# Kernel optimization log

Hardware: AMD Instinct MI355X
Metric: run time of the kernel (lower is better)

## Reference

```python
import jax, jax.numpy as jnp
import numpy as np

IN_F, OUT_F, N_PAIRS, BATCH = 1024, 1024, 4096, 32768
EPS = 1e-5

def setup_inputs() -> dict:
    key = jax.random.key(0)
    ks = jax.random.split(key, 8)
    x = jax.random.normal(ks[0], (BATCH, IN_F), dtype=jnp.float32)
    idx_i = jax.random.randint(ks[1], (N_PAIRS,), 0, IN_F)
    idx_j = jax.random.randint(ks[2], (N_PAIRS,), 0, IN_F)
    bound_lc = 1.0 / np.sqrt(N_PAIRS)
    bound_w1 = 1.0 / np.sqrt(IN_F)
    lw = jax.random.uniform(ks[3], (OUT_F, N_PAIRS), minval=-bound_lc, maxval=bound_lc, dtype=jnp.float32)
    w1 = jax.random.uniform(ks[4], (OUT_F, IN_F), minval=-bound_w1, maxval=bound_w1, dtype=jnp.float32)
    scale = jnp.ones((1, IN_F), dtype=jnp.float32)
    translation = jnp.zeros((1, IN_F), dtype=jnp.float32)
    gamma = jnp.ones((OUT_F,), dtype=jnp.float32)
    beta = jnp.zeros((OUT_F,), dtype=jnp.float32)
    return {"x": x, "idx_i": idx_i, "idx_j": idx_j, "scale": scale,
            "translation": translation, "lw": lw, "w1": w1,
            "gamma": gamma, "beta": beta}

def reference(x, idx_i, idx_j, scale, translation, lw, w1, gamma, beta):
    # levicivita transform: affine-normalize, gather pairs, multiply, GEMM
    xs = (x - translation) / scale                       # [B, in]
    pp = xs[:, idx_i] * xs[:, idx_j]                     # [B, num_pairs]
    lc = pp @ lw.T                                       # [B, out]
    base = x @ w1.T                                      # [B, out]
    c = lc + base
    # LayerNorm over last dim (eps=1e-5, biased variance, as torch)
    mu = jnp.mean(c, axis=-1, keepdims=True)
    var = jnp.mean(jnp.square(c - mu), axis=-1, keepdims=True)
    return (c - mu) * jax.lax.rsqrt(var + EPS) * gamma + beta
```

## Files before the change

kernel.cpp:

```cpp
#include <hip/hip_runtime.h>
#include <hip/hip_bf16.h>
#include <stdint.h>


#define IN_F 1024
#define OUT_F 1024
#define N_PAIRS 4096
#define BATCH_N 32768
#define KTOT (N_PAIRS + IN_F)
#define EPS_LN 1e-5f

#define BM 256
#define BN 256
#define BK 64
#define NKT (KTOT / BK)
#define RS ((size_t)KTOT * 2)

typedef __attribute__((ext_vector_type(8))) __bf16 bf16x8;
typedef __attribute__((ext_vector_type(4))) float f32x4;

__device__ __forceinline__ unsigned short f32_to_bf16_bits(float f) {
  union { float f; unsigned u; } c; c.f = f;
  unsigned r = c.u + 0x7FFFu + ((c.u >> 16) & 1u);
  return (unsigned short)(r >> 16);
}

__device__ __forceinline__ void gload_lds16(const void* g, void* l) {
  __builtin_amdgcn_global_load_lds(
      (const __attribute__((address_space(1))) void*)g,
      (__attribute__((address_space(3))) void*)l, 16, 0, 0);
}

__global__ __launch_bounds__(256) void prep_w_kernel(
    const float* __restrict__ lw, const float* __restrict__ w1,
    unsigned short* __restrict__ Wcat) {
  int t = blockIdx.x * 256 + threadIdx.x;
  int e = t * 4;
  int o = e / KTOT;
  int k = e - o * KTOT;
  const float* src = (k < N_PAIRS) ? (lw + (size_t)o * N_PAIRS + k)
                                   : (w1 + (size_t)o * IN_F + (k - N_PAIRS));
  float4 v = *reinterpret_cast<const float4*>(src);
  ushort4 b;
  b.x = f32_to_bf16_bits(v.x);
  b.y = f32_to_bf16_bits(v.y);
  b.z = f32_to_bf16_bits(v.z);
  b.w = f32_to_bf16_bits(v.w);
  *reinterpret_cast<ushort4*>(Wcat + e) = b;
}

__global__ __launch_bounds__(256) void prep_x_kernel(
    const float* __restrict__ x,
    const int* __restrict__ idx_i, const int* __restrict__ idx_j,
    const float* __restrict__ scale, const float* __restrict__ translation,
    unsigned short* __restrict__ Xcat, int rowBase) {
  __shared__ float xs[IN_F];
  int r = blockIdx.x;
  int t = threadIdx.x;
  const float* xrow = x + (size_t)(rowBase + r) * IN_F;
  float4 xv = reinterpret_cast<const float4*>(xrow)[t];
  float4 sv = reinterpret_cast<const float4*>(scale)[t];
  float4 tv = reinterpret_cast<const float4*>(translation)[t];
  float4 xsv;
  xsv.x = (xv.x - tv.x) / sv.x;
  xsv.y = (xv.y - tv.y) / sv.y;
  xsv.z = (xv.z - tv.z) / sv.z;
  xsv.w = (xv.w - tv.w) / sv.w;
  reinterpret_cast<float4*>(xs)[t] = xsv;

  unsigned short* rowout = Xcat + (size_t)r * KTOT;
  ushort4 xb;
  xb.x = f32_to_bf16_bits(xv.x);
  xb.y = f32_to_bf16_bits(xv.y);
  xb.z = f32_to_bf16_bits(xv.z);
  xb.w = f32_to_bf16_bits(xv.w);
  *reinterpret_cast<ushort4*>(rowout + N_PAIRS + t * 4) = xb;

  __syncthreads();
#pragma unroll
  for (int g = 0; g < 2; ++g) {
    int p = (g * 256 + t) * 8;
    int4 ia = *reinterpret_cast<const int4*>(idx_i + p);
    int4 ib = *reinterpret_cast<const int4*>(idx_i + p + 4);
    int4 ja = *reinterpret_cast<const int4*>(idx_j + p);
    int4 jb = *reinterpret_cast<const int4*>(idx_j + p + 4);
    ushort4 oa, ob;
    oa.x = f32_to_bf16_bits(xs[ia.x] * xs[ja.x]);
    oa.y = f32_to_bf16_bits(xs[ia.y] * xs[ja.y]);
    oa.z = f32_to_bf16_bits(xs[ia.z] * xs[ja.z]);
    oa.w = f32_to_bf16_bits(xs[ia.w] * xs[ja.w]);
    ob.x = f32_to_bf16_bits(xs[ib.x] * xs[jb.x]);
    ob.y = f32_to_bf16_bits(xs[ib.y] * xs[jb.y]);
    ob.z = f32_to_bf16_bits(xs[ib.z] * xs[jb.z]);
    ob.w = f32_to_bf16_bits(xs[ib.w] * xs[jb.w]);
    *reinterpret_cast<ushort4*>(rowout + p) = oa;
    *reinterpret_cast<ushort4*>(rowout + p + 4) = ob;
  }
}


#define STAGE_HALF(h_)                                                        \
  {                                                                           \
    int h__ = (h_);                                                           \
    if (h__ < 4 * NKT) {                                                      \
      int kt__ = h__ >> 2, rg__ = h__ & 3;                                    \
      const char* mb__ = (rg__ < 2) ? Bb : Ab;                                \
      const char* src__ = mb__ + (size_t)((rg__ & 1) * 128 + srow) * RS +     \
                          (size_t)kt__ * 128 + skb;                           \
      char* dst__ = lds + ((kt__ & 1) << 16) + (rg__ << 14) + (w << 10);      \
      gload_lds16(src__, dst__);                                              \
      gload_lds16(src__ + (size_t)64 * RS, dst__ + 8192);                     \
    }                                                                         \
  }

#define PHASE_SYNC()                                                          \
  __builtin_amdgcn_sched_barrier(0);                                          \
  __builtin_amdgcn_s_barrier();                                               \
  asm volatile("s_waitcnt lgkmcnt(0)" ::: "memory");                          \
  __builtin_amdgcn_sched_barrier(0);

#define PHASE_END()                                                           \
  __builtin_amdgcn_sched_barrier(0);                                          \
  __builtin_amdgcn_s_barrier();                                               \
  __builtin_amdgcn_sched_barrier(0);

#define MFMA_PAIR(mb)                                                         \
  __builtin_amdgcn_s_setprio(1);                                              \
  _Pragma("unroll") for (int i_ = 0; i_ < 2; ++i_)                            \
      _Pragma("unroll") for (int n_ = 0; n_ < 4; ++n_) {                      \
    acc[(mb) + i_][n_] = __builtin_amdgcn_mfma_f32_16x16x32_bf16(             \
        am[(mb) + i_][0], bfr[n_][0], acc[(mb) + i_][n_], 0, 0, 0);           \
    acc[(mb) + i_][n_] = __builtin_amdgcn_mfma_f32_16x16x32_bf16(             \
        am[(mb) + i_][1], bfr[n_][1], acc[(mb) + i_][n_], 0, 0, 0);           \
  }                                                                           \
  __builtin_amdgcn_s_setprio(0);

__global__ __launch_bounds__(512, 2) void gemm_kernel(
    const unsigned short* __restrict__ A,
    const unsigned short* __restrict__ Bw,
    float* __restrict__ C) {
  __shared__ __align__(16) char lds[131072];

  int nwg = gridDim.x;
  int bid = blockIdx.x;
  int cpx = nwg >> 3;
  int swz = (bid & 7) * cpx + (bid >> 3);
  int rt = swz >> 2;
  int ct = swz & 3;

  int tid = threadIdx.x;
  int lane = tid & 63;
  int w = tid >> 6;
  int wr = w >> 2;
  int wc = w & 3;

  const char* Ab = (const char*)A + (size_t)rt * BM * RS;
  const char* Bb = (const char*)Bw + (size_t)ct * BN * RS;

  int srow = tid >> 3;
  int skb = ((tid & 7) << 4) ^ (((tid >> 3) & 7) << 4);

  int lane15 = lane & 15;
  int cb = lane >> 4;
  int swzm = (lane15 & 7) << 4;
  int kb0 = (cb << 4) ^ swzm;
  int kb1 = (64 + (cb << 4)) ^ swzm;
  const char* aRow = lds + 32768 + (wr * 128 + lane15) * 128;
  const char* bRow = lds + (wc * 64 + lane15) * 128;

  f32x4 acc[8][4];
#pragma unroll
  for (int m = 0; m < 8; ++m)
#pragma unroll
    for (int n = 0; n < 4; ++n) acc[m][n] = {0.f, 0.f, 0.f, 0.f};

#pragma unroll
  for (int hp = 0; hp < 7; ++hp) {
    STAGE_HALF(hp);
    __builtin_amdgcn_sched_barrier(0);
  }
  asm volatile("s_waitcnt vmcnt(6)" ::: "memory");
  __builtin_amdgcn_s_barrier();
  __builtin_amdgcn_sched_barrier(0);

  for (int kt = 0; kt < NKT; ++kt) {
    int bo = (kt & 1) << 16;
    bf16x8 bfr[4][2], am[8][2];

#pragma unroll
    for (int n = 0; n < 4; ++n) {
      bfr[n][0] = *(const bf16x8*)(bRow + bo + n * 2048 + kb0);
      bfr[n][1] = *(const bf16x8*)(bRow + bo + n * 2048 + kb1);
    }
#pragma unroll
    for (int m = 0; m < 2; ++m) {
      am[m][0] = *(const bf16x8*)(aRow + bo + m * 2048 + kb0);
      am[m][1] = *(const bf16x8*)(aRow + bo + m * 2048 + kb1);
    }
    STAGE_HALF(4 * kt + 7);
    PHASE_SYNC();
    MFMA_PAIR(0);
    PHASE_END();

#pragma unroll
    for (int m = 2; m < 4; ++m) {
      am[m][0] = *(const bf16x8*)(aRow + bo + m * 2048 + kb0);
      am[m][1] = *(const bf16x8*)(aRow + bo + m * 2048 + kb1);
    }
    STAGE_HALF(4 * kt + 8);
    PHASE_SYNC();
    MFMA_PAIR(2);
    PHASE_END();

#pragma unroll
    for (int m = 4; m < 8; ++m) {
      am[m][0] = *(const bf16x8*)(aRow + bo + m * 2048 + kb0);
      am[m][1] = *(const bf16x8*)(aRow + bo + m * 2048 + kb1);
    }
    STAGE_HALF(4 * kt + 9);
    PHASE_SYNC();
    MFMA_PAIR(4);
    PHASE_END();

    STAGE_HALF(4 * kt + 10);
    PHASE_SYNC();
    MFMA_PAIR(6);
    __builtin_amdgcn_sched_barrier(0);
    if (kt + 2 < NKT) {
      asm volatile("s_waitcnt vmcnt(6)" ::: "memory");
    } else if (kt + 1 < NKT) {
      asm volatile("s_waitcnt vmcnt(0)" ::: "memory");
    }
    __builtin_amdgcn_s_barrier();
    __builtin_amdgcn_sched_barrier(0);
  }

  int crow0 = rt * BM + wr * 128 + (cb << 2);
  int ccol0 = ct * BN + wc * 64 + lane15;
#pragma unroll
  for (int m = 0; m < 8; ++m)
#pragma unroll
    for (int n = 0; n < 4; ++n)
#pragma unroll
      for (int j = 0; j < 4; ++j)
        C[(size_t)(crow0 + m * 16 + j) * OUT_F + ccol0 + n * 16] = acc[m][n][j];
}

__global__ __launch_bounds__(256) void ln_kernel(
    float* __restrict__ C, const float* __restrict__ gamma,
    const float* __restrict__ beta) {
  int r = blockIdx.x;
  int t = threadIdx.x;
  float* row = C + (size_t)r * OUT_F;
  float4 v = reinterpret_cast<const float4*>(row)[t];
  float s = v.x + v.y + v.z + v.w;
  float s2 = v.x * v.x + v.y * v.y + v.z * v.z + v.w * v.w;
#pragma unroll
  for (int off = 32; off > 0; off >>= 1) {
    s += __shfl_down(s, off, 64);
    s2 += __shfl_down(s2, off, 64);
  }
  __shared__ float ps[4], ps2[4];
  int lane = t & 63, wid = t >> 6;
  if (lane == 0) { ps[wid] = s; ps2[wid] = s2; }
  __syncthreads();
  float fs = ps[0] + ps[1] + ps[2] + ps[3];
  float fs2 = ps2[0] + ps2[1] + ps2[2] + ps2[3];
  float mu = fs * (1.0f / OUT_F);
  float var = fs2 * (1.0f / OUT_F) - mu * mu;
  float rstd = rsqrtf(var + EPS_LN);
  float4 g = reinterpret_cast<const float4*>(gamma)[t];
  float4 b = reinterpret_cast<const float4*>(beta)[t];
  float4 o;
  o.x = (v.x - mu) * rstd * g.x + b.x;
  o.y = (v.y - mu) * rstd * g.y + b.y;
  o.z = (v.z - mu) * rstd * g.z + b.z;
  o.w = (v.w - mu) * rstd * g.w + b.w;
  reinterpret_cast<float4*>(row)[t] = o;
}

extern "C" void kernel_launch(void* const* d_in, const int* in_sizes, int n_in,
                              void* d_out, int out_size, void* d_ws, size_t ws_size,
                              hipStream_t stream) {
  const float* x           = (const float*)d_in[0];
  const int*   idx_i       = (const int*)d_in[1];
  const int*   idx_j       = (const int*)d_in[2];
  const float* scale       = (const float*)d_in[3];
  const float* translation = (const float*)d_in[4];
  const float* lw          = (const float*)d_in[5];
  const float* w1          = (const float*)d_in[6];
  const float* gamma       = (const float*)d_in[7];
  const float* beta        = (const float*)d_in[8];
  float* out = (float*)d_out;

  unsigned short* Wcat = (unsigned short*)d_ws;
  size_t wcat_bytes = (size_t)OUT_F * KTOT * 2;
  unsigned short* Xcat = (unsigned short*)((char*)d_ws + wcat_bytes);
  size_t avail = ws_size > wcat_bytes ? ws_size - wcat_bytes : 0;

  int chunk = BATCH_N;
  while (chunk > 512 && (size_t)chunk * KTOT * 2 > avail) chunk >>= 1;

  prep_w_kernel<<<dim3(OUT_F * KTOT / 4 / 256), dim3(256), 0, stream>>>(lw, w1, Wcat);

  for (int rb = 0; rb < BATCH_N; rb += chunk) {
    prep_x_kernel<<<dim3(chunk), dim3(256), 0, stream>>>(
        x, idx_i, idx_j, scale, translation, Xcat, rb);
    gemm_kernel<<<dim3((chunk / BM) * (OUT_F / BN)), dim3(512), 0, stream>>>(
        Xcat, Wcat, out + (size_t)rb * OUT_F);
  }

  ln_kernel<<<dim3(BATCH_N), dim3(256), 0, stream>>>(out, gamma, beta);
}
```

Before: 446.0 us.

## Restructure GEMM k-loop into half-K phases and store bf16 intermediate for LayerNorm

Reorganizes the GEMM main loop so each K tile is processed in four phases split by K-half and M-half. This cuts the barriers per tile and reuses the B fragments across M halves, with staging prefetch reordered to match (6 stages in flight instead of 7). The GEMM output is now written as bf16 to a workspace buffer, and LayerNorm reads it per chunk and writes the final fp32 output. This halves the intermediate write and read traffic but rounds the pre-norm activations to bf16, which loses some accuracy.

After: 426.0 us. 4.5% less time.

```diff
diff --git a/kernel.cpp b/kernel.cpp
--- a/kernel.cpp
+++ b/kernel.cpp
@@ -23,6 +23,11 @@
   union { float f; unsigned u; } c; c.f = f;
   unsigned r = c.u + 0x7FFFu + ((c.u >> 16) & 1u);
   return (unsigned short)(r >> 16);
+}
+
+__device__ __forceinline__ float bf16_bits_to_f32(unsigned short b) {
+  union { unsigned u; float f; } c; c.u = ((unsigned)b) << 16;
+  return c.f;
 }
 
 __device__ __forceinline__ void gload_lds16(const void* g, void* l) {
@@ -113,32 +118,21 @@
     }                                                                         \
   }
 
-#define PHASE_SYNC()                                                          \
-  __builtin_amdgcn_sched_barrier(0);                                          \
-  __builtin_amdgcn_s_barrier();                                               \
-  asm volatile("s_waitcnt lgkmcnt(0)" ::: "memory");                          \
-  __builtin_amdgcn_sched_barrier(0);
-
-#define PHASE_END()                                                           \
-  __builtin_amdgcn_sched_barrier(0);                                          \
-  __builtin_amdgcn_s_barrier();                                               \
-  __builtin_amdgcn_sched_barrier(0);
-
-#define MFMA_PAIR(mb)                                                         \
+#define SB0() __builtin_amdgcn_sched_barrier(0)
+#define LGKM0() asm volatile("s_waitcnt lgkmcnt(0)" ::: "memory")
+
+#define MFMA_Q(mb, amv, bv)                                                   \
   __builtin_amdgcn_s_setprio(1);                                              \
-  _Pragma("unroll") for (int i_ = 0; i_ < 2; ++i_)                            \
-      _Pragma("unroll") for (int n_ = 0; n_ < 4; ++n_) {                      \
+  _Pragma("unroll") for (int i_ = 0; i_ < 4; ++i_)                            \
+      _Pragma("unroll") for (int n_ = 0; n_ < 4; ++n_)                        \
     acc[(mb) + i_][n_] = __builtin_amdgcn_mfma_f32_16x16x32_bf16(             \
-        am[(mb) + i_][0], bfr[n_][0], acc[(mb) + i_][n_], 0, 0, 0);           \
-    acc[(mb) + i_][n_] = __builtin_amdgcn_mfma_f32_16x16x32_bf16(             \
-        am[(mb) + i_][1], bfr[n_][1], acc[(mb) + i_][n_], 0, 0, 0);           \
-  }                                                                           \
+        amv[i_], bv[n_], acc[(mb) + i_][n_], 0, 0, 0);                        \
   __builtin_amdgcn_s_setprio(0);
 
 __global__ __launch_bounds__(512, 2) void gemm_kernel(
     const unsigned short* __restrict__ A,
     const unsigned short* __restrict__ Bw,
-    float* __restrict__ C) {
+    unsigned short* __restrict__ Cb) {
   __shared__ __align__(16) char lds[131072];
 
   int nwg = gridDim.x;
@@ -175,64 +169,66 @@
     for (int n = 0; n < 4; ++n) acc[m][n] = {0.f, 0.f, 0.f, 0.f};
 
 #pragma unroll
-  for (int hp = 0; hp < 7; ++hp) {
+  for (int hp = 0; hp < 6; ++hp) {
     STAGE_HALF(hp);
-    __builtin_amdgcn_sched_barrier(0);
-  }
-  asm volatile("s_waitcnt vmcnt(6)" ::: "memory");
+    SB0();
+  }
+  asm volatile("s_waitcnt vmcnt(4)" ::: "memory");
   __builtin_amdgcn_s_barrier();
-  __builtin_amdgcn_sched_barrier(0);
+  SB0();
 
   for (int kt = 0; kt < NKT; ++kt) {
     int bo = (kt & 1) << 16;
-    bf16x8 bfr[4][2], am[8][2];
-
-#pragma unroll
-    for (int n = 0; n < 4; ++n) {
-      bfr[n][0] = *(const bf16x8*)(bRow + bo + n * 2048 + kb0);
-      bfr[n][1] = *(const bf16x8*)(bRow + bo + n * 2048 + kb1);
-    }
-#pragma unroll
-    for (int m = 0; m < 2; ++m) {
-      am[m][0] = *(const bf16x8*)(aRow + bo + m * 2048 + kb0);
-      am[m][1] = *(const bf16x8*)(aRow + bo + m * 2048 + kb1);
-    }
-    STAGE_HALF(4 * kt + 7);
-    PHASE_SYNC();
-    MFMA_PAIR(0);
-    PHASE_END();
-
-#pragma unroll
-    for (int m = 2; m < 4; ++m) {
-      am[m][0] = *(const bf16x8*)(aRow + bo + m * 2048 + kb0);
-      am[m][1] = *(const bf16x8*)(aRow + bo + m * 2048 + kb1);
-    }
-    STAGE_HALF(4 * kt + 8);
-    PHASE_SYNC();
-    MFMA_PAIR(2);
-    PHASE_END();
-
-#pragma unroll
-    for (int m = 4; m < 8; ++m) {
-      am[m][0] = *(const bf16x8*)(aRow + bo + m * 2048 + kb0);
-      am[m][1] = *(const bf16x8*)(aRow + bo + m * 2048 + kb1);
-    }
-    STAGE_HALF(4 * kt + 9);
-    PHASE_SYNC();
-    MFMA_PAIR(4);
-    PHASE_END();
-
-    STAGE_HALF(4 * kt + 10);
-    PHASE_SYNC();
-    MFMA_PAIR(6);
-    __builtin_amdgcn_sched_barrier(0);
+    bf16x8 bf0[4], bf1[4], a0[4], a1[4], a2[4], a3[4];
+
+#pragma unroll
+    for (int n = 0; n < 4; ++n) bf0[n] = *(const bf16x8*)(bRow + bo + n * 2048 + kb0);
+#pragma unroll
+    for (int i = 0; i < 4; ++i) a0[i] = *(const bf16x8*)(aRow + bo + i * 2048 + kb0);
+    LGKM0();
+    SB0();
+    MFMA_Q(0, a0, bf0);
+#pragma unroll
+    for (int n = 0; n < 4; ++n) bf1[n] = *(const bf16x8*)(bRow + bo + n * 2048 + kb1);
+#pragma unroll
+    for (int i = 0; i < 4; ++i) a1[i] = *(const bf16x8*)(aRow + bo + i * 2048 + kb1);
+    STAGE_HALF(4 * (kt + 1) + 2);
+    SB0();
+    __builtin_amdgcn_s_barrier();
+    SB0();
+
+    LGKM0();
+    SB0();
+    MFMA_Q(0, a1, bf1);
+#pragma unroll
+    for (int i = 0; i < 4; ++i) a2[i] = *(const bf16x8*)(aRow + bo + (4 + i) * 2048 + kb0);
+    STAGE_HALF(4 * (kt + 1) + 3);
+    SB0();
+    __builtin_amdgcn_s_barrier();
+    SB0();
+
+    LGKM0();
+    SB0();
+    MFMA_Q(4, a2, bf0);
+#pragma unroll
+    for (int i = 0; i < 4; ++i) a3[i] = *(const bf16x8*)(aRow + bo + (4 + i) * 2048 + kb1);
+    STAGE_HALF(4 * (kt + 2) + 0);
+    SB0();
+    __builtin_amdgcn_s_barrier();
+    SB0();
+
+    LGKM0();
+    SB0();
+    MFMA_Q(4, a3, bf1);
+    STAGE_HALF(4 * (kt + 2) + 1);
+    SB0();
     if (kt + 2 < NKT) {
-      asm volatile("s_waitcnt vmcnt(6)" ::: "memory");
+      asm volatile("s_waitcnt vmcnt(4)" ::: "memory");
     } else if (kt + 1 < NKT) {
       asm volatile("s_waitcnt vmcnt(0)" ::: "memory");
     }
     __builtin_amdgcn_s_barrier();
-    __builtin_amdgcn_sched_barrier(0);
+    SB0();
   }
 
   int crow0 = rt * BM + wr * 128 + (cb << 2);
@@ -243,16 +239,21 @@
     for (int n = 0; n < 4; ++n)
 #pragma unroll
       for (int j = 0; j < 4; ++j)
-        C[(size_t)(crow0 + m * 16 + j) * OUT_F + ccol0 + n * 16] = acc[m][n][j];
+        Cb[(size_t)(crow0 + m * 16 + j) * OUT_F + ccol0 + n * 16] =
+            f32_to_bf16_bits(acc[m][n][j]);
 }
 
 __global__ __launch_bounds__(256) void ln_kernel(
-    float* __restrict__ C, const float* __restrict__ gamma,
-    const float* __restrict__ beta) {
+    const unsigned short* __restrict__ Cb, float* __restrict__ out,
+    const float* __restrict__ gamma, const float* __restrict__ beta) {
   int r = blockIdx.x;
   int t = threadIdx.x;
-  float* row = C + (size_t)r * OUT_F;
-  float4 v = reinterpret_cast<const float4*>(row)[t];
+  ushort4 u = reinterpret_cast<const ushort4*>(Cb + (size_t)r * OUT_F)[t];
+  float4 v;
+  v.x = bf16_bits_to_f32(u.x);
+  v.y = bf16_bits_to_f32(u.y);
+  v.z = bf16_bits_to_f32(u.z);
+  v.w = bf16_bits_to_f32(u.w);
   float s = v.x + v.y + v.z + v.w;
   float s2 = v.x * v.x + v.y * v.y + v.z * v.z + v.w * v.w;
 #pragma unroll
@@ -276,7 +277,7 @@
   o.y = (v.y - mu) * rstd * g.y + b.y;
   o.z = (v.z - mu) * rstd * g.z + b.z;
   o.w = (v.w - mu) * rstd * g.w + b.w;
-  reinterpret_cast<float4*>(row)[t] = o;
+  reinterpret_cast<float4*>(out + (size_t)r * OUT_F)[t] = o;
 }
 
 extern "C" void kernel_launch(void* const* d_in, const int* in_sizes, int n_in,
@@ -295,11 +296,13 @@
 
   unsigned short* Wcat = (unsigned short*)d_ws;
   size_t wcat_bytes = (size_t)OUT_F * KTOT * 2;
-  unsigned short* Xcat = (unsigned short*)((char*)d_ws + wcat_bytes);
   size_t avail = ws_size > wcat_bytes ? ws_size - wcat_bytes : 0;
 
   int chunk = BATCH_N;
-  while (chunk > 512 && (size_t)chunk * KTOT * 2 > avail) chunk >>= 1;
+  while (chunk > 512 && (size_t)chunk * (KTOT * 2 + OUT_F * 2) > avail) chunk >>= 1;
+
+  unsigned short* Cb = (unsigned short*)((char*)d_ws + wcat_bytes);
+  unsigned short* Xcat = Cb + (size_t)chunk * OUT_F;
 
   prep_w_kernel<<<dim3(OUT_F * KTOT / 4 / 256), dim3(256), 0, stream>>>(lw, w1, Wcat);
 
@@ -307,8 +310,8 @@
     prep_x_kernel<<<dim3(chunk), dim3(256), 0, stream>>>(
         x, idx_i, idx_j, scale, translation, Xcat, rb);
     gemm_kernel<<<dim3((chunk / BM) * (OUT_F / BN)), dim3(512), 0, stream>>>(
-        Xcat, Wcat, out + (size_t)rb * OUT_F);
-  }
-
-  ln_kernel<<<dim3(BATCH_N), dim3(256), 0, stream>>>(out, gamma, beta);
-}
+        Xcat, Wcat, Cb);
+    ln_kernel<<<dim3(chunk), dim3(256), 0, stream>>>(
+        Cb, out + (size_t)rb * OUT_F, gamma, beta);
+  }
+}
```
